# Kernel tuning notes

Hardware: AMD Instinct MI355X
Metric: run time of the kernel (lower is better)

## Reference

```python
import jax, jax.numpy as jnp
import numpy as np

B, C, H, NP, M = 32, 768, 12, 196, 64
D = C // H
GRID = 14  # sqrt(196)
NG = 1 + NP  # cls + patches = 197
EPS = 1e-5


def _ln(x, w, b):
    mu = x.mean(-1, keepdims=True)
    var = ((x - mu) ** 2).mean(-1, keepdims=True)
    return (x - mu) * jax.lax.rsqrt(var + EPS) * w + b


def setup_inputs() -> dict:
    key = jax.random.key(0)
    ks = jax.random.split(key, 14)
    std = 0.02
    return {
        "x": jax.random.normal(ks[0], (B, NG + M, C), dtype=jnp.float32),
        "ps": jax.random.uniform(ks[1], (B, M, 2), dtype=jnp.float32) * 224.0,
        "ns": jax.random.randint(ks[2], (B,), 1, M + 1, dtype=jnp.int32),
        "norm1_w": jnp.ones((C,), jnp.float32),
        "norm1_b": jnp.zeros((C,), jnp.float32),
        "qkv_w": jax.random.normal(ks[3], (3 * C, C), jnp.float32) * std,
        "proj_w": jax.random.normal(ks[4], (C, C), jnp.float32) * std,
        "proj_b": jnp.zeros((C,), jnp.float32),
        "norm2_w": jnp.ones((C,), jnp.float32),
        "norm2_b": jnp.zeros((C,), jnp.float32),
        "fc1_w": jax.random.normal(ks[5], (4 * C, C), jnp.float32) * std,
        "fc1_b": jnp.zeros((4 * C,), jnp.float32),
        "fc2_w": jax.random.normal(ks[6], (C, 4 * C), jnp.float32) * std,
        "fc2_b": jnp.zeros((C,), jnp.float32),
    }


def reference(x, ps, ns, norm1_w, norm1_b, qkv_w, proj_w, proj_b,
              norm2_w, norm2_b, fc1_w, fc1_b, fc2_w, fc2_b):
    Bn, Nt, Cd = x.shape  # Nt = 1 + 196 + M
    scale = D ** -0.5

    h = _ln(x, norm1_w, norm1_b)
    qkv = (h @ qkv_w.T).reshape(Bn, Nt, 3, H, D).transpose(2, 0, 3, 1, 4)  # [3,B,H,Nt,D]
    q, k, v = qkv[0], qkv[1], qkv[2]

    # ---- global attention over cls + patch tokens (first 197) ----
    attn = jnp.einsum('bhnd,bhmd->bhnm', q[:, :, :NG], k[:, :, :NG]) * scale
    attn = jax.nn.softmax(attn, axis=-1)
    xg = jnp.einsum('bhnm,bhmd->bhnd', attn, v[:, :, :NG])
    xg = xg.transpose(0, 2, 1, 3).reshape(Bn, NG, Cd)  # [B,197,C]

    # ---- keypoint bilinear-gather attention (get_single_filter_matrix) ----
    pos = ps / 16.0  # [B,M,2]; pos[...,1] -> row (dim 4), pos[...,0] -> col (dim 5)
    c0 = jnp.clip(jnp.floor(pos[..., 0]), 0, GRID - 1).astype(jnp.int32)
    c1 = jnp.clip(jnp.ceil(pos[..., 0]), 0, GRID - 1).astype(jnp.int32)
    r0 = jnp.clip(jnp.floor(pos[..., 1]), 0, GRID - 1).astype(jnp.int32)
    r1 = jnp.clip(jnp.ceil(pos[..., 1]), 0, GRID - 1).astype(jnp.int32)
    # neighbor order: top_left, top_right, bottom_left, bottom_right
    rows = jnp.stack([r0, r1, r0, r1], axis=-1)  # [B,M,4]
    cols = jnp.stack([c0, c0, c1, c1], axis=-1)
    flat = rows * GRID + cols  # [B,M,4] flat index into 196 patch tokens

    kp = k[:, :, 1:NG]  # [B,H,196,D]
    vp = v[:, :, 1:NG]
    idx = jnp.broadcast_to(flat.reshape(Bn, 1, M * 4, 1), (Bn, H, M * 4, D))
    knb = jnp.take_along_axis(kp, idx, axis=2).reshape(Bn, H, M, 4, D)
    vnb = jnp.take_along_axis(vp, idx, axis=2).reshape(Bn, H, M, 4, D)

    qk = q[:, :, NG:]  # keypoint queries [B,H,M,D]
    a = jnp.einsum('bhmd,bhmjd->bhmj', qk, knb)  # no scale, per original
    a = jax.nn.softmax(a, axis=-1)
    kout = jnp.einsum('bhmj,bhmjd->bhmd', a, vnb)
    kout = kout.transpose(0, 2, 1, 3).reshape(Bn, M, Cd)

    y = jnp.concatenate([xg, kout], axis=1) @ proj_w.T + proj_b
    x = x + y

    h2 = _ln(x, norm2_w, norm2_b)
    h2 = jax.nn.gelu(h2 @ fc1_w.T + fc1_b, approximate=False)
    x = x + (h2 @ fc2_w.T + fc2_b)
    return x
```

## Files before the change

### kernel.cpp

```cpp
#include <hip/hip_runtime.h>

typedef unsigned short u16;
typedef unsigned int u32;
typedef u16 u16x8 __attribute__((ext_vector_type(8)));
typedef u16 u16x4 __attribute__((ext_vector_type(4)));
typedef float f32x4 __attribute__((ext_vector_type(4)));
typedef __bf16 bf16x8 __attribute__((ext_vector_type(8)));

#define NHEAD 12
#define NT 261
#define NGL 197
#define CDIM 768
#define KT 14
#define PS_STRIDE 232
#define VT_STRIDE 232

__device__ __forceinline__ float bf2f(u16 u) {
    u32 x = ((u32)u) << 16;
    float f;
    __builtin_memcpy(&f, &x, 4);
    return f;
}
__device__ __forceinline__ u16 f2bf(float f) {
    u32 x;
    __builtin_memcpy(&x, &f, 4);
    x = (x + 0x7fffu + ((x >> 16) & 1u)) >> 16;
    return (u16)x;
}

#define GLD_LDS16(g, l) \
    __builtin_amdgcn_global_load_lds((const __attribute__((address_space(1))) void*)(g), \
                                     (__attribute__((address_space(3))) void*)(l), 16, 0, 0)
#define WAITV(n) asm volatile("s_waitcnt vmcnt(" #n ")" ::: "memory")
#define BARM() asm volatile("s_barrier" ::: "memory")

struct CvArgs {
    const float* in[4];
    u16* out[4];
    int n4[4];
};

__device__ __forceinline__ void ln_row(const float* __restrict__ in, const float* __restrict__ w,
                                       const float* __restrict__ bia, u16* __restrict__ out,
                                       int row, int lane) {
    const float4* r = (const float4*)(in + (size_t)row * CDIM);
    float4 a = r[lane], b4 = r[lane + 64], c4 = r[lane + 128];
    float s  = a.x + a.y + a.z + a.w + b4.x + b4.y + b4.z + b4.w + c4.x + c4.y + c4.z + c4.w;
    float ss = a.x*a.x + a.y*a.y + a.z*a.z + a.w*a.w
             + b4.x*b4.x + b4.y*b4.y + b4.z*b4.z + b4.w*b4.w
             + c4.x*c4.x + c4.y*c4.y + c4.z*c4.z + c4.w*c4.w;
#pragma unroll
    for (int off = 32; off; off >>= 1) {
        s  += __shfl_xor(s, off);
        ss += __shfl_xor(ss, off);
    }
    float mu = s * (1.f / 768.f);
    float var = ss * (1.f / 768.f) - mu * mu;
    float inv = rsqrtf(var + 1e-5f);
    const float4* wp = (const float4*)w;
    const float4* bp = (const float4*)bia;
    u16* o = out + (size_t)row * CDIM;
#pragma unroll
    for (int t = 0; t < 3; ++t) {
        float4 v = (t == 0) ? a : (t == 1) ? b4 : c4;
        float4 ww = wp[lane + t * 64], bb = bp[lane + t * 64];
        u16x4 ov;
        ov[0] = f2bf((v.x - mu) * inv * ww.x + bb.x);
        ov[1] = f2bf((v.y - mu) * inv * ww.y + bb.y);
        ov[2] = f2bf((v.z - mu) * inv * ww.z + bb.z);
        ov[3] = f2bf((v.w - mu) * inv * ww.w + bb.w);
        *(u16x4*)(o + t * 256 + lane * 4) = ov;
    }
}

__global__ __launch_bounds__(256) void pre_k(const float* __restrict__ x, const float* __restrict__ w,
                                             const float* __restrict__ bia, u16* __restrict__ out,
                                             int nrows, CvArgs cv) {
    if (blockIdx.y == 0) {
        int i = blockIdx.x * 256 + threadIdx.x;
        int s0 = cv.n4[0], s1 = s0 + cv.n4[1], s2 = s1 + cv.n4[2], s3 = s2 + cv.n4[3];
        const float* in;
        u16* o;
        int base;
        if (i < s0)      { in = cv.in[0]; o = cv.out[0]; base = 0; }
        else if (i < s1) { in = cv.in[1]; o = cv.out[1]; base = s0; }
        else if (i < s2) { in = cv.in[2]; o = cv.out[2]; base = s1; }
        else if (i < s3) { in = cv.in[3]; o = cv.out[3]; base = s2; }
        else return;
        int j = i - base;
        float4 v = ((const float4*)in)[j];
        u16x4 ov;
        ov[0] = f2bf(v.x); ov[1] = f2bf(v.y); ov[2] = f2bf(v.z); ov[3] = f2bf(v.w);
        ((u16x4*)o)[j] = ov;
    } else {
        int lane = threadIdx.x & 63, wv = threadIdx.x >> 6;
        int row = blockIdx.x * 4 + wv;
        if (row < nrows) ln_row(x, w, bia, out, row, lane);
    }
}

__global__ __launch_bounds__(256) void ln_w(const float* __restrict__ in, const float* __restrict__ w,
                                            const float* __restrict__ bia, u16* __restrict__ out, int nrows) {
    int lane = threadIdx.x & 63, wv = threadIdx.x >> 6;
    int row = blockIdx.x * 4 + wv;
    if (row < nrows) ln_row(in, w, bia, out, row, lane);
}

template <int EPI>
__global__ __launch_bounds__(512, 2) void gemm5(const u16* __restrict__ A, const u16* __restrict__ Bw,
                                                int M, int N, int K, int nbn,
                                                const float* __restrict__ bias,
                                                void* __restrict__ outp) {
    __shared__ __align__(16) u16 sm[2][32768];
    const int tid = threadIdx.x;
    const int nwg = gridDim.x;
    const int q = nwg >> 3, r = nwg & 7;
    const int xcd = blockIdx.x & 7, within = blockIdx.x >> 3;
    const int id2 = (xcd < r ? xcd * (q + 1) : r * (q + 1) + (xcd - r) * q) + within;
    const int bm = id2 / nbn, bn = id2 % nbn;
    const int lane = tid & 63, wv = tid >> 6;
    const int wr = wv >> 2, wc = wv & 3;
    const int l15 = lane & 15, lg = lane >> 4;
    const int arow0 = bm * 256, brow0 = bn * 256;
    const int nt = K >> 6;

    const int srow = tid >> 3;
    const int sk = ((tid & 7) ^ (srow & 7)) * 8;
    const u16* gA[4];
    const u16* gB[4];
#pragma unroll
    for (int i = 0; i < 4; ++i) {
        int ar = arow0 + i * 64 + srow;
        if (ar >= M) ar = M - 1;
        gA[i] = A + (size_t)ar * K + sk;
        gB[i] = Bw + (size_t)(brow0 + i * 64 + srow) * K + sk;
    }

    auto STAGE = [&](int tt) {
        u16* sb = sm[tt & 1];
        const size_t ko = (size_t)tt * 64;
#pragma unroll
        for (int i = 0; i < 4; ++i) GLD_LDS16(gA[i] + ko, sb + i * 4096 + tid * 8);
#pragma unroll
        for (int i = 0; i < 4; ++i) GLD_LDS16(gB[i] + ko, sb + 16384 + i * 4096 + tid * 8);
    };

    f32x4 acc[8][4] = {};
    const int xb = l15 & 7;

    STAGE(0);
    for (int t = 0; t < nt; ++t) {
        if (t + 1 < nt) {
            STAGE(t + 1);
            WAITV(8);
        } else {
            WAITV(0);
        }
        BARM();
        const u16* sb = sm[t & 1];
        bf16x8 bq[4][2];
#pragma unroll
        for (int ni = 0; ni < 4; ++ni)
#pragma unroll
            for (int kk = 0; kk < 2; ++kk)
                bq[ni][kk] = *(const bf16x8*)(sb + 16384 + (wc * 64 + ni * 16 + l15) * 64 + (((kk << 2) | lg) ^ xb) * 8);
#pragma unroll
        for (int mi = 0; mi < 8; ++mi) {
            const u16* arow = sb + (wr * 128 + mi * 16 + l15) * 64;
            bf16x8 a0 = *(const bf16x8*)(arow + ((lg ^ xb) * 8));
            bf16x8 a1 = *(const bf16x8*)(arow + (((4 | lg) ^ xb) * 8));
#pragma unroll
            for (int ni = 0; ni < 4; ++ni) {
                acc[mi][ni] = __builtin_amdgcn_mfma_f32_16x16x32_bf16(a0, bq[ni][0], acc[mi][ni], 0, 0, 0);
                acc[mi][ni] = __builtin_amdgcn_mfma_f32_16x16x32_bf16(a1, bq[ni][1], acc[mi][ni], 0, 0, 0);
            }
        }
        if (t + 2 < nt) BARM();
    }

#pragma unroll
    for (int mi = 0; mi < 8; ++mi) {
        int row0 = arow0 + wr * 128 + mi * 16 + lg * 4;
#pragma unroll
        for (int ni = 0; ni < 4; ++ni) {
            int col = brow0 + wc * 64 + ni * 16 + l15;
            float bb = (EPI == 0) ? 0.f : bias[col];
#pragma unroll
            for (int rr = 0; rr < 4; ++rr) {
                int row = row0 + rr;
                if (row < M) {
                    float v = acc[mi][ni][rr] + bb;
                    if (EPI == 2) {
                        float z = v + 0.044715f * v * v * v;
                        v = v / (1.f + __expf(-1.5957691216f * z));
                    }
                    ((u16*)outp)[(size_t)row * N + col] = f2bf(v);
                }
            }
        }
    }
}

__global__ __launch_bounds__(256, 2) void gemm4n(const u16* __restrict__ A, const u16* __restrict__ Bw,
                                                 int M, int N, int K, int nbn,
                                                 const float* __restrict__ bias,
                                                 const float* __restrict__ resid, void* __restrict__ outp) {
    constexpr int SLOT = 128 * 64 + 8192;
    __shared__ __align__(16) u16 sm[2 * SLOT];
    const int tid = threadIdx.x;
    const int nwg = gridDim.x;
    const int q = nwg >> 3, r = nwg & 7;
    const int xcd = blockIdx.x & 7, within = blockIdx.x >> 3;
    const int id2 = (xcd < r ? xcd * (q + 1) : r * (q + 1) + (xcd - r) * q) + within;
    const int bm = id2 / nbn, bn = id2 % nbn;
    const int lane = tid & 63, wv = tid >> 6;
    const int wr = wv >> 1, wc = wv & 1;
    const int l15 = lane & 15, lg = lane >> 4;
    const int arow0 = bm * 128, brow0 = bn * 128;
    const int nt = K >> 6;

    const int srow = tid >> 3;
    const int sk = ((tid & 7) ^ (srow & 7)) * 8;
    const u16* gA[4];
    const u16* gB[4];
#pragma unroll
    for (int i = 0; i < 4; ++i) {
        int ar = arow0 + i * 32 + srow;
        if (ar >= M) ar = M - 1;
        gA[i] = A + (size_t)ar * K + sk;
        gB[i] = Bw + (size_t)(brow0 + i * 32 + srow) * K + sk;
    }

    auto STAGE = [&](int tt) {
        u16* sb = sm + (tt & 1) * SLOT;
        const size_t ko = (size_t)tt * 64;
#pragma unroll
        for (int i = 0; i < 4; ++i) GLD_LDS16(gA[i] + ko, sb + i * 2048 + tid * 8);
#pragma unroll
        for (int i = 0; i < 4; ++i) GLD_LDS16(gB[i] + ko, sb + 8192 + i * 2048 + tid * 8);
    };

    f32x4 acc[4][4] = {};
    const int xb = l15 & 7;

    STAGE(0);
    for (int t = 0; t < nt; ++t) {
        if (t + 1 < nt) {
            STAGE(t + 1);
            WAITV(8);
        } else {
            WAITV(0);
        }
        BARM();
        const u16* sb = sm + (t & 1) * SLOT;
        bf16x8 af[4][2], bq[4][2];
#pragma unroll
        for (int mi = 0; mi < 4; ++mi)
#pragma unroll
            for (int kk = 0; kk < 2; ++kk)
                af[mi][kk] = *(const bf16x8*)(sb + (wr * 64 + mi * 16 + l15) * 64 + (((kk << 2) | lg) ^ xb) * 8);
#pragma unroll
        for (int ni = 0; ni < 4; ++ni)
#pragma unroll
            for (int kk = 0; kk < 2; ++kk)
                bq[ni][kk] = *(const bf16x8*)(sb + 8192 + (wc * 64 + ni * 16 + l15) * 64 + (((kk << 2) | lg) ^ xb) * 8);
#pragma unroll
        for (int mi = 0; mi < 4; ++mi)
#pragma unroll
            for (int ni = 0; ni < 4; ++ni) {
                acc[mi][ni] = __builtin_amdgcn_mfma_f32_16x16x32_bf16(af[mi][0], bq[ni][0], acc[mi][ni], 0, 0, 0);
                acc[mi][ni] = __builtin_amdgcn_mfma_f32_16x16x32_bf16(af[mi][1], bq[ni][1], acc[mi][ni], 0, 0, 0);
            }
        if (t + 2 < nt) BARM();
    }

#pragma unroll
    for (int mi = 0; mi < 4; ++mi) {
        int row0 = arow0 + wr * 64 + mi * 16 + lg * 4;
#pragma unroll
        for (int ni = 0; ni < 4; ++ni) {
            int col = brow0 + wc * 64 + ni * 16 + l15;
            float bb = bias[col];
#pragma unroll
            for (int rr = 0; rr < 4; ++rr) {
                int row = row0 + rr;
                if (row < M) {
                    float v = acc[mi][ni][rr] + bb + resid[(size_t)row * N + col];
                    ((float*)outp)[(size_t)row * N + col] = v;
                }
            }
        }
    }
}

__global__ __launch_bounds__(256) void attn_fused(const u16* __restrict__ qkv, const float* __restrict__ ps,
                                                  u16* __restrict__ Z) {
    __shared__ __align__(16) u16 lds0[4 * 16 * PS_STRIDE];
    __shared__ __align__(16) u16 Vt[64 * VT_STRIDE];
    const int tid = threadIdx.x;
    const int lane = tid & 63, wv = tid >> 6;

    if (blockIdx.x >= 1536) {
        int idx = blockIdx.x - 1536;
        int b = idx >> 4;
        int m = (idx & 15) * 4 + wv;
        float px = ps[((size_t)b * 64 + m) * 2 + 0] * (1.f / 16.f);
        float py = ps[((size_t)b * 64 + m) * 2 + 1] * (1.f / 16.f);
        int c0 = min(max((int)floorf(px), 0), 13);
        int c1 = min(max((int)ceilf(px), 0), 13);
        int r0 = min(max((int)floorf(py), 0), 13);
        int r1 = min(max((int)ceilf(py), 0), 13);
        int tok[4];
        tok[0] = 1 + r0 * 14 + c0;
        tok[1] = 1 + r1 * 14 + c0;
        tok[2] = 1 + r0 * 14 + c1;
        tok[3] = 1 + r1 * 14 + c1;
        const size_t rowq = ((size_t)b * NT + NGL + m) * 2304;
#pragma unroll 1
        for (int h = 0; h < NHEAD; ++h) {
            float qv = bf2f(qkv[rowq + h * 64 + lane]);
            float a[4];
#pragma unroll
            for (int j = 0; j < 4; ++j) {
                float p = qv * bf2f(qkv[((size_t)b * NT + tok[j]) * 2304 + 768 + h * 64 + lane]);
#pragma unroll
                for (int off = 32; off; off >>= 1) p += __shfl_xor(p, off);
                a[j] = p;
            }
            float mx = fmaxf(fmaxf(a[0], a[1]), fmaxf(a[2], a[3]));
            float e0 = expf(a[0] - mx), e1 = expf(a[1] - mx), e2 = expf(a[2] - mx), e3 = expf(a[3] - mx);
            float inv = 1.f / (e0 + e1 + e2 + e3);
            float v0 = bf2f(qkv[((size_t)b * NT + tok[0]) * 2304 + 1536 + h * 64 + lane]);
            float v1 = bf2f(qkv[((size_t)b * NT + tok[1]) * 2304 + 1536 + h * 64 + lane]);
            float v2 = bf2f(qkv[((size_t)b * NT + tok[2]) * 2304 + 1536 + h * 64 + lane]);
            float v3 = bf2f(qkv[((size_t)b * NT + tok[3]) * 2304 + 1536 + h * 64 + lane]);
            float o = (e0 * v0 + e1 * v1 + e2 * v2 + e3 * v3) * inv;
            Z[((size_t)b * NT + NGL + m) * CDIM + h * 64 + lane] = f2bf(o);
        }
        return;
    }

    const int blk = blockIdx.x;
    const int qt = blk & 3;
    const int bh = blk >> 2;
    const int h = bh % NHEAD, b = bh / NHEAD;
    const int l15 = lane & 15, lg = lane >> 4;
    const u16* base = qkv + (size_t)b * NT * 2304;

    for (int c = tid; c < 224 * 8; c += 256) {
        int row = c >> 3, ch = c & 7;
        u16x8 v = {};
        if (row < NGL) v = *(const u16x8*)(base + (size_t)row * 2304 + 768 + h * 64 + ch * 8);
        int byte = row * 128 + ((ch * 16) ^ ((row & 7) << 4));
        *(u16x8*)((char*)lds0 + byte) = v;
    }
    for (int c = tid; c < 112 * 8; c += 256) {
        int mp = c >> 3, dch = c & 7;
        int m0 = mp * 2;
        u16x8 a0 = {}, a1 = {};
        if (m0 < NGL)     a0 = *(const u16x8*)(base + (size_t)m0 * 2304 + 1536 + h * 64 + dch * 8);
        if (m0 + 1 < NGL) a1 = *(const u16x8*)(base + (size_t)(m0 + 1) * 2304 + 1536 + h * 64 + dch * 8);
#pragma unroll
        for (int j = 0; j < 8; ++j) {
            u32 pk = (u32)a0[j] | ((u32)a1[j] << 16);
            *(u32*)((char*)Vt + (size_t)(dch * 8 + j) * (VT_STRIDE * 2) + m0 * 2) = pk;
        }
    }
    const int q0 = qt * 64 + wv * 16;
    int qrow = q0 + l15; if (qrow > NGL - 1) qrow = NGL - 1;
    bf16x8 aq0 = *(const bf16x8*)(base + (size_t)qrow * 2304 + h * 64 + lg * 8);
    bf16x8 aq1 = *(const bf16x8*)(base + (size_t)qrow * 2304 + h * 64 + 32 + lg * 8);
    __syncthreads();

    f32x4 s[KT];
    const int sw = (l15 & 7) << 4;
#pragma unroll
    for (int t = 0; t < KT; ++t) {
        const char* krow = (const char*)lds0 + (t * 16 + l15) * 128;
        bf16x8 bk0 = *(const bf16x8*)(krow + ((lg * 16) ^ sw));
        bf16x8 bk1 = *(const bf16x8*)(krow + ((64 + lg * 16) ^ sw));
        f32x4 acc = {};
        acc = __builtin_amdgcn_mfma_f32_16x16x32_bf16(aq0, bk0, acc, 0, 0, 0);
        acc = __builtin_amdgcn_mfma_f32_16x16x32_bf16(aq1, bk1, acc, 0, 0, 0);
        s[t] = acc * 0.125f;
    }
    float mx[4] = {-1e30f, -1e30f, -1e30f, -1e30f};
#pragma unroll
    for (int t = 0; t < KT; ++t)
#pragma unroll
        for (int r = 0; r < 4; ++r) mx[r] = fmaxf(mx[r], s[t][r]);
#pragma unroll
    for (int off = 1; off < 16; off <<= 1)
#pragma unroll
        for (int r = 0; r < 4; ++r) mx[r] = fmaxf(mx[r], __shfl_xor(mx[r], off));
    float sum[4] = {};
#pragma unroll
    for (int t = 0; t < KT; ++t) {
        bool valid = (t * 16 + l15) < NGL;
#pragma unroll
        for (int r = 0; r < 4; ++r) {
            float e = valid ? __expf(s[t][r] - mx[r]) : 0.f;
            s[t][r] = e;
            sum[r] += e;
        }
    }
#pragma unroll
    for (int off = 1; off < 16; off <<= 1)
#pragma unroll
        for (int r = 0; r < 4; ++r) sum[r] += __shfl_xor(sum[r], off);
    float inv[4];
#pragma unroll
    for (int r = 0; r < 4; ++r) inv[r] = 1.f / sum[r];

    __syncthreads();
    u16* Pw = lds0 + wv * 16 * PS_STRIDE;
#pragma unroll
    for (int t = 0; t < KT; ++t)
#pragma unroll
        for (int r = 0; r < 4; ++r)
            Pw[(4 * lg + r) * PS_STRIDE + t * 16 + l15] = f2bf(s[t][r] * inv[r]);

    f32x4 o[4] = {};
#pragma unroll
    for (int ks = 0; ks < 7; ++ks) {
        bf16x8 pa = *(const bf16x8*)(Pw + l15 * PS_STRIDE + ks * 32 + lg * 8);
#pragma unroll
        for (int dt = 0; dt < 4; ++dt) {
            bf16x8 bv = *(const bf16x8*)((const char*)Vt + (size_t)(dt * 16 + l15) * (VT_STRIDE * 2) + ks * 64 + lg * 16);
            o[dt] = __builtin_amdgcn_mfma_f32_16x16x32_bf16(pa, bv, o[dt], 0, 0, 0);
        }
    }
#pragma unroll
    for (int dt = 0; dt < 4; ++dt)
#pragma unroll
        for (int r = 0; r < 4; ++r) {
            int q = q0 + 4 * lg + r;
            if (q < NGL) Z[((size_t)b * NT + q) * CDIM + h * 64 + dt * 16 + l15] = f2bf(o[dt][r]);
        }
}

extern "C" void kernel_launch(void* const* d_in, const int* in_sizes, int n_in,
                              void* d_out, int out_size, void* d_ws, size_t ws_size,
                              hipStream_t stream) {
    const float* x      = (const float*)d_in[0];
    const float* ps     = (const float*)d_in[1];
    const float* n1w    = (const float*)d_in[3];
    const float* n1b    = (const float*)d_in[4];
    const float* qkv_w  = (const float*)d_in[5];
    const float* proj_w = (const float*)d_in[6];
    const float* proj_b = (const float*)d_in[7];
    const float* n2w    = (const float*)d_in[8];
    const float* n2b    = (const float*)d_in[9];
    const float* fc1_w  = (const float*)d_in[10];
    const float* fc1_b  = (const float*)d_in[11];
    const float* fc2_w  = (const float*)d_in[12];
    const float* fc2_b  = (const float*)d_in[13];

    char* ws = (char*)d_ws;
    const int M = 32 * NT;
    u16* hbuf  = (u16*)ws;
    u16* qkvb  = (u16*)(ws + 12828672);
    u16* Zb    = (u16*)(ws + 12828672 + 38486016);
    u16* Gb    = (u16*)(ws + 12828672);
    float* x1  = (float*)(ws + 64143360);
    u16* wq    = (u16*)(ws + 89800704);
    u16* wp    = wq + 2304 * 768;
    u16* w1    = wp + 768 * 768;
    u16* w2    = w1 + 3072 * 768;

    CvArgs cv;
    cv.in[0] = qkv_w;  cv.out[0] = wq; cv.n4[0] = 2304 * 768 / 4;
    cv.in[1] = proj_w; cv.out[1] = wp; cv.n4[1] = 768 * 768 / 4;
    cv.in[2] = fc1_w;  cv.out[2] = w1; cv.n4[2] = 3072 * 768 / 4;
    cv.in[3] = fc2_w;  cv.out[3] = w2; cv.n4[3] = 768 * 3072 / 4;

    pre_k<<<dim3(6912, 2), 256, 0, stream>>>(x, n1w, n1b, hbuf, M, cv);
    gemm5<0><<<33 * 9, 512, 0, stream>>>(hbuf, wq, M, 2304, 768, 9, nullptr, qkvb);
    attn_fused<<<2048, 256, 0, stream>>>(qkvb, ps, Zb);
    gemm4n<<<66 * 6, 256, 0, stream>>>(Zb, wp, M, 768, 768, 6, proj_b, x, x1);
    ln_w<<<2088, 256, 0, stream>>>(x1, n2w, n2b, hbuf, M);
    gemm5<2><<<33 * 12, 512, 0, stream>>>(hbuf, w1, M, 3072, 768, 12, fc1_b, Gb);
    gemm4n<<<66 * 6, 256, 0, stream>>>(Gb, w2, M, 768, 3072, 6, fc2_b, x1, (float*)d_out);
}
```

Baseline: 302.0 us.

## Split GEMM main loop into four interleaved load/MFMA phases with priority hints

Restructures the 256x256 bf16 GEMM main loop into four quadrant phases. Each phase issues a slice of the next tile's global-to-LDS loads, reads part of the A/B fragments from LDS, and runs a quarter of the MFMAs under raised wave priority. The aim is to spread memory traffic across the compute and overlap LDS reads with MFMA work, in the style of ping-pong scheduling. The cost is many more barriers per iteration, and the finer-grained waits could serialize warps if the phases are unbalanced.

```diff
diff --git a/kernel.cpp b/kernel.cpp
--- a/kernel.cpp
+++ b/kernel.cpp
@@ -32,6 +32,7 @@
     __builtin_amdgcn_global_load_lds((const __attribute__((address_space(1))) void*)(g), \
                                      (__attribute__((address_space(3))) void*)(l), 16, 0, 0)
 #define WAITV(n) asm volatile("s_waitcnt vmcnt(" #n ")" ::: "memory")
+#define LGKM0() do { asm volatile("s_waitcnt lgkmcnt(0)" ::: "memory"); __builtin_amdgcn_sched_barrier(0); } while (0)
 #define BARM() asm volatile("s_barrier" ::: "memory")
 
 struct CvArgs {
@@ -107,7 +108,7 @@
 }
 
 template <int EPI>
-__global__ __launch_bounds__(512, 2) void gemm5(const u16* __restrict__ A, const u16* __restrict__ Bw,
+__global__ __launch_bounds__(512, 2) void gemm8(const u16* __restrict__ A, const u16* __restrict__ Bw,
                                                 int M, int N, int K, int nbn,
                                                 const float* __restrict__ bias,
                                                 void* __restrict__ outp) {
@@ -136,46 +137,114 @@
         gB[i] = Bw + (size_t)(brow0 + i * 64 + srow) * K + sk;
     }
 
-    auto STAGE = [&](int tt) {
-        u16* sb = sm[tt & 1];
-        const size_t ko = (size_t)tt * 64;
-#pragma unroll
-        for (int i = 0; i < 4; ++i) GLD_LDS16(gA[i] + ko, sb + i * 4096 + tid * 8);
-#pragma unroll
-        for (int i = 0; i < 4; ++i) GLD_LDS16(gB[i] + ko, sb + 16384 + i * 4096 + tid * 8);
-    };
-
     f32x4 acc[8][4] = {};
     const int xb = l15 & 7;
-
-    STAGE(0);
+    const int lds_tid = tid * 8;
+
+    {
+        u16* nb = sm[0];
+#pragma unroll
+        for (int i = 0; i < 4; ++i) GLD_LDS16(gA[i], nb + i * 4096 + lds_tid);
+#pragma unroll
+        for (int i = 0; i < 4; ++i) GLD_LDS16(gB[i], nb + 16384 + i * 4096 + lds_tid);
+    }
+
     for (int t = 0; t < nt; ++t) {
-        if (t + 1 < nt) {
-            STAGE(t + 1);
-            WAITV(8);
+        const u16* sb = sm[t & 1];
+        u16* nb = sm[(t & 1) ^ 1];
+        const bool pre = (t + 1 < nt);
+        const size_t ko = (size_t)(t + 1) * 64;
+        bf16x8 aLo[4][2], aHi[4][2], bLo[2][2], bHi[2][2];
+
+        if (pre) {
+            GLD_LDS16(gA[0] + ko, nb + 0 * 4096 + lds_tid);
+            GLD_LDS16(gA[1] + ko, nb + 1 * 4096 + lds_tid);
+            WAITV(2);
         } else {
             WAITV(0);
         }
         BARM();
-        const u16* sb = sm[t & 1];
-        bf16x8 bq[4][2];
-#pragma unroll
-        for (int ni = 0; ni < 4; ++ni)
+#pragma unroll
+        for (int mi = 0; mi < 4; ++mi)
 #pragma unroll
             for (int kk = 0; kk < 2; ++kk)
-                bq[ni][kk] = *(const bf16x8*)(sb + 16384 + (wc * 64 + ni * 16 + l15) * 64 + (((kk << 2) | lg) ^ xb) * 8);
-#pragma unroll
-        for (int mi = 0; mi < 8; ++mi) {
-            const u16* arow = sb + (wr * 128 + mi * 16 + l15) * 64;
-            bf16x8 a0 = *(const bf16x8*)(arow + ((lg ^ xb) * 8));
-            bf16x8 a1 = *(const bf16x8*)(arow + (((4 | lg) ^ xb) * 8));
-#pragma unroll
-            for (int ni = 0; ni < 4; ++ni) {
-                acc[mi][ni] = __builtin_amdgcn_mfma_f32_16x16x32_bf16(a0, bq[ni][0], acc[mi][ni], 0, 0, 0);
-                acc[mi][ni] = __builtin_amdgcn_mfma_f32_16x16x32_bf16(a1, bq[ni][1], acc[mi][ni], 0, 0, 0);
-            }
-        }
-        if (t + 2 < nt) BARM();
+                aLo[mi][kk] = *(const bf16x8*)(sb + (wr * 128 + mi * 16 + l15) * 64 + (((kk << 2) | lg) ^ xb) * 8);
+#pragma unroll
+        for (int ni = 0; ni < 2; ++ni)
+#pragma unroll
+            for (int kk = 0; kk < 2; ++kk)
+                bLo[ni][kk] = *(const bf16x8*)(sb + 16384 + (wc * 64 + ni * 16 + l15) * 64 + (((kk << 2) | lg) ^ xb) * 8);
+        LGKM0();
+        __builtin_amdgcn_s_setprio(1);
+#pragma unroll
+        for (int mi = 0; mi < 4; ++mi)
+#pragma unroll
+            for (int ni = 0; ni < 2; ++ni) {
+                acc[mi][ni] = __builtin_amdgcn_mfma_f32_16x16x32_bf16(aLo[mi][0], bLo[ni][0], acc[mi][ni], 0, 0, 0);
+                acc[mi][ni] = __builtin_amdgcn_mfma_f32_16x16x32_bf16(aLo[mi][1], bLo[ni][1], acc[mi][ni], 0, 0, 0);
+            }
+        __builtin_amdgcn_s_setprio(0);
+        BARM();
+
+        if (pre) {
+            GLD_LDS16(gA[2] + ko, nb + 2 * 4096 + lds_tid);
+            GLD_LDS16(gA[3] + ko, nb + 3 * 4096 + lds_tid);
+        }
+#pragma unroll
+        for (int ni = 0; ni < 2; ++ni)
+#pragma unroll
+            for (int kk = 0; kk < 2; ++kk)
+                bHi[ni][kk] = *(const bf16x8*)(sb + 16384 + (wc * 64 + (ni + 2) * 16 + l15) * 64 + (((kk << 2) | lg) ^ xb) * 8);
+        BARM();
+        LGKM0();
+        __builtin_amdgcn_s_setprio(1);
+#pragma unroll
+        for (int mi = 0; mi < 4; ++mi)
+#pragma unroll
+            for (int ni = 0; ni < 2; ++ni) {
+                acc[mi][ni + 2] = __builtin_amdgcn_mfma_f32_16x16x32_bf16(aLo[mi][0], bHi[ni][0], acc[mi][ni + 2], 0, 0, 0);
+                acc[mi][ni + 2] = __builtin_amdgcn_mfma_f32_16x16x32_bf16(aLo[mi][1], bHi[ni][1], acc[mi][ni + 2], 0, 0, 0);
+            }
+        __builtin_amdgcn_s_setprio(0);
+        BARM();
+
+        if (pre) {
+            GLD_LDS16(gB[0] + ko, nb + 16384 + 0 * 4096 + lds_tid);
+            GLD_LDS16(gB[1] + ko, nb + 16384 + 1 * 4096 + lds_tid);
+        }
+#pragma unroll
+        for (int mi = 0; mi < 4; ++mi)
+#pragma unroll
+            for (int kk = 0; kk < 2; ++kk)
+                aHi[mi][kk] = *(const bf16x8*)(sb + (wr * 128 + (mi + 4) * 16 + l15) * 64 + (((kk << 2) | lg) ^ xb) * 8);
+        BARM();
+        LGKM0();
+        __builtin_amdgcn_s_setprio(1);
+#pragma unroll
+        for (int mi = 0; mi < 4; ++mi)
+#pragma unroll
+            for (int ni = 0; ni < 2; ++ni) {
+                acc[mi + 4][ni + 2] = __builtin_amdgcn_mfma_f32_16x16x32_bf16(aHi[mi][0], bHi[ni][0], acc[mi + 4][ni + 2], 0, 0, 0);
+                acc[mi + 4][ni + 2] = __builtin_amdgcn_mfma_f32_16x16x32_bf16(aHi[mi][1], bHi[ni][1], acc[mi + 4][ni + 2], 0, 0, 0);
+            }
+        __builtin_amdgcn_s_setprio(0);
+        BARM();
+
+        if (pre) {
+            GLD_LDS16(gB[2] + ko, nb + 16384 + 2 * 4096 + lds_tid);
+            GLD_LDS16(gB[3] + ko, nb + 16384 + 3 * 4096 + lds_tid);
+        }
+        BARM();
+        __builtin_amdgcn_s_setprio(1);
+#pragma unroll
+        for (int mi = 0; mi < 4; ++mi)
+#pragma unroll
+            for (int ni = 0; ni < 2; ++ni) {
+                acc[mi + 4][ni] = __builtin_amdgcn_mfma_f32_16x16x32_bf16(aHi[mi][0], bLo[ni][0], acc[mi + 4][ni], 0, 0, 0);
+                acc[mi + 4][ni] = __builtin_amdgcn_mfma_f32_16x16x32_bf16(aHi[mi][1], bLo[ni][1], acc[mi + 4][ni], 0, 0, 0);
+            }
+        __builtin_amdgcn_s_setprio(0);
+        BARM();
     }
 
 #pragma unroll
@@ -475,10 +544,10 @@
     cv.in[3] = fc2_w;  cv.out[3] = w2; cv.n4[3] = 768 * 3072 / 4;
 
     pre_k<<<dim3(6912, 2), 256, 0, stream>>>(x, n1w, n1b, hbuf, M, cv);
-    gemm5<0><<<33 * 9, 512, 0, stream>>>(hbuf, wq, M, 2304, 768, 9, nullptr, qkvb);
+    gemm8<0><<<33 * 9, 512, 0, stream>>>(hbuf, wq, M, 2304, 768, 9, nullptr, qkvb);
     attn_fused<<<2048, 256, 0, stream>>>(qkvb, ps, Zb);
     gemm4n<<<66 * 6, 256, 0, stream>>>(Zb, wp, M, 768, 768, 6, proj_b, x, x1);
     ln_w<<<2088, 256, 0, stream>>>(x1, n2w, n2b, hbuf, M);
-    gemm5<2><<<33 * 12, 512, 0, stream>>>(hbuf, w1, M, 3072, 768, 12, fc1_b, Gb);
+    gemm8<2><<<33 * 12, 512, 0, stream>>>(hbuf, w1, M, 3072, 768, 12, fc1_b, Gb);
     gemm4n<<<66 * 6, 256, 0, stream>>>(Gb, w2, M, 768, 3072, 6, fc2_b, x1, (float*)d_out);
 }
```

New measurement: 301.9 us. No clear change (-0.0%).

## Pre-pack weights into MFMA fragment layout and load B directly to registers

Applied to the files above, without the earlier changes.

The weight conversion kernel now writes bf16 weights in a tiled layout that matches the 16x32 MFMA B-fragment. All four GEMMs then load B fragments straight from global memory into registers, so only A is staged through LDS. The main loop is unrolled by two with register double-buffering of B. This cuts LDS traffic and LDS footprint, but each wave now loads B independently from global or L2, so the same B data is fetched more times. It also adds a scheduling barrier after each vmcnt wait.

```diff
diff --git a/kernel.cpp b/kernel.cpp
--- a/kernel.cpp
+++ b/kernel.cpp
@@ -27,17 +27,23 @@
     x = (x + 0x7fffu + ((x >> 16) & 1u)) >> 16;
     return (u16)x;
 }
+__device__ __forceinline__ bf16x8 asbf(u16x8 v) {
+    bf16x8 r;
+    __builtin_memcpy(&r, &v, 16);
+    return r;
+}
 
 #define GLD_LDS16(g, l) \
     __builtin_amdgcn_global_load_lds((const __attribute__((address_space(1))) void*)(g), \
                                      (__attribute__((address_space(3))) void*)(l), 16, 0, 0)
-#define WAITV(n) asm volatile("s_waitcnt vmcnt(" #n ")" ::: "memory")
+#define WAITV(n) do { asm volatile("s_waitcnt vmcnt(" #n ")" ::: "memory"); __builtin_amdgcn_sched_barrier(0); } while (0)
 #define BARM() asm volatile("s_barrier" ::: "memory")
 
 struct CvArgs {
     const float* in[4];
     u16* out[4];
-    int n4[4];
+    int n8[4];
+    int K[4];
 };
 
 __device__ __forceinline__ void ln_row(const float* __restrict__ in, const float* __restrict__ w,
@@ -78,20 +84,27 @@
                                              int nrows, CvArgs cv) {
     if (blockIdx.y == 0) {
         int i = blockIdx.x * 256 + threadIdx.x;
-        int s0 = cv.n4[0], s1 = s0 + cv.n4[1], s2 = s1 + cv.n4[2], s3 = s2 + cv.n4[3];
-        const float* in;
-        u16* o;
-        int base;
-        if (i < s0)      { in = cv.in[0]; o = cv.out[0]; base = 0; }
-        else if (i < s1) { in = cv.in[1]; o = cv.out[1]; base = s0; }
-        else if (i < s2) { in = cv.in[2]; o = cv.out[2]; base = s1; }
-        else if (i < s3) { in = cv.in[3]; o = cv.out[3]; base = s2; }
+        int s0 = cv.n8[0], s1 = s0 + cv.n8[1], s2 = s1 + cv.n8[2], s3 = s2 + cv.n8[3];
+        int seg, base;
+        if (i < s0)      { seg = 0; base = 0; }
+        else if (i < s1) { seg = 1; base = s0; }
+        else if (i < s2) { seg = 2; base = s1; }
+        else if (i < s3) { seg = 3; base = s2; }
         else return;
         int j = i - base;
-        float4 v = ((const float4*)in)[j];
-        u16x4 ov;
-        ov[0] = f2bf(v.x); ov[1] = f2bf(v.y); ov[2] = f2bf(v.z); ov[3] = f2bf(v.w);
-        ((u16x4*)o)[j] = ov;
+        int Kd = cv.K[seg];
+        int kd8 = Kd >> 3;
+        int n = j / kd8;
+        int k8 = j - n * kd8;
+        const float* src = cv.in[seg] + (size_t)n * Kd + k8 * 8;
+        float4 v0 = *(const float4*)src;
+        float4 v1 = *(const float4*)(src + 4);
+        u16x8 ov;
+        ov[0] = f2bf(v0.x); ov[1] = f2bf(v0.y); ov[2] = f2bf(v0.z); ov[3] = f2bf(v0.w);
+        ov[4] = f2bf(v1.x); ov[5] = f2bf(v1.y); ov[6] = f2bf(v1.z); ov[7] = f2bf(v1.w);
+        int chunk = (n >> 4) * (Kd >> 5) + (k8 >> 2);
+        int dst = chunk * 512 + ((k8 & 3) * 16 + (n & 15)) * 8;
+        *(u16x8*)(cv.out[seg] + dst) = ov;
     } else {
         int lane = threadIdx.x & 63, wv = threadIdx.x >> 6;
         int row = blockIdx.x * 4 + wv;
@@ -107,11 +120,10 @@
 }
 
 template <int EPI>
-__global__ __launch_bounds__(512, 2) void gemm5(const u16* __restrict__ A, const u16* __restrict__ Bw,
-                                                int M, int N, int K, int nbn,
-                                                const float* __restrict__ bias,
-                                                void* __restrict__ outp) {
-    __shared__ __align__(16) u16 sm[2][32768];
+__global__ __launch_bounds__(512) void gemm9(const u16* __restrict__ A, const u16* __restrict__ Bp,
+                                             int M, int N, int K, int nbn,
+                                             const float* __restrict__ bias, void* __restrict__ outp) {
+    __shared__ __align__(16) u16 smA[2][16384];
     const int tid = threadIdx.x;
     const int nwg = gridDim.x;
     const int q = nwg >> 3, r = nwg & 7;
@@ -123,47 +135,38 @@
     const int l15 = lane & 15, lg = lane >> 4;
     const int arow0 = bm * 256, brow0 = bn * 256;
     const int nt = K >> 6;
+    const int kch = K >> 5;
 
     const int srow = tid >> 3;
     const int sk = ((tid & 7) ^ (srow & 7)) * 8;
     const u16* gA[4];
-    const u16* gB[4];
 #pragma unroll
     for (int i = 0; i < 4; ++i) {
         int ar = arow0 + i * 64 + srow;
         if (ar >= M) ar = M - 1;
         gA[i] = A + (size_t)ar * K + sk;
-        gB[i] = Bw + (size_t)(brow0 + i * 64 + srow) * K + sk;
-    }
-
-    auto STAGE = [&](int tt) {
-        u16* sb = sm[tt & 1];
+    }
+    const u16* gBw = Bp + ((size_t)((brow0 >> 4) + wc * 4)) * kch * 512 + lane * 8;
+
+    auto STAGE_A = [&](int tt) {
+        u16* sb = smA[tt & 1];
         const size_t ko = (size_t)tt * 64;
 #pragma unroll
         for (int i = 0; i < 4; ++i) GLD_LDS16(gA[i] + ko, sb + i * 4096 + tid * 8);
-#pragma unroll
-        for (int i = 0; i < 4; ++i) GLD_LDS16(gB[i] + ko, sb + 16384 + i * 4096 + tid * 8);
     };
 
     f32x4 acc[8][4] = {};
     const int xb = l15 & 7;
-
-    STAGE(0);
-    for (int t = 0; t < nt; ++t) {
-        if (t + 1 < nt) {
-            STAGE(t + 1);
-            WAITV(8);
-        } else {
-            WAITV(0);
-        }
-        BARM();
-        const u16* sb = sm[t & 1];
-        bf16x8 bq[4][2];
+    u16x8 BqA[8], BqB[8];
+
+    auto LOADB = [&](u16x8* dst, int tt) {
 #pragma unroll
         for (int ni = 0; ni < 4; ++ni)
 #pragma unroll
             for (int kk = 0; kk < 2; ++kk)
-                bq[ni][kk] = *(const bf16x8*)(sb + 16384 + (wc * 64 + ni * 16 + l15) * 64 + (((kk << 2) | lg) ^ xb) * 8);
+                dst[ni * 2 + kk] = *(const u16x8*)(gBw + ((size_t)ni * kch + 2 * tt + kk) * 512);
+    };
+    auto COMPUTE = [&](const u16* sb, const u16x8* Bq) {
 #pragma unroll
         for (int mi = 0; mi < 8; ++mi) {
             const u16* arow = sb + (wr * 128 + mi * 16 + l15) * 64;
@@ -171,11 +174,34 @@
             bf16x8 a1 = *(const bf16x8*)(arow + (((4 | lg) ^ xb) * 8));
 #pragma unroll
             for (int ni = 0; ni < 4; ++ni) {
-                acc[mi][ni] = __builtin_amdgcn_mfma_f32_16x16x32_bf16(a0, bq[ni][0], acc[mi][ni], 0, 0, 0);
-                acc[mi][ni] = __builtin_amdgcn_mfma_f32_16x16x32_bf16(a1, bq[ni][1], acc[mi][ni], 0, 0, 0);
+                acc[mi][ni] = __builtin_amdgcn_mfma_f32_16x16x32_bf16(a0, asbf(Bq[ni * 2]), acc[mi][ni], 0, 0, 0);
+                acc[mi][ni] = __builtin_amdgcn_mfma_f32_16x16x32_bf16(a1, asbf(Bq[ni * 2 + 1]), acc[mi][ni], 0, 0, 0);
             }
         }
-        if (t + 2 < nt) BARM();
+    };
+
+    STAGE_A(0);
+    LOADB(BqA, 0);
+    for (int t = 0; t < nt; t += 2) {
+        STAGE_A(t + 1);
+        LOADB(BqB, t + 1);
+        WAITV(12);
+        BARM();
+        COMPUTE(smA[0], BqA);
+        if (t + 2 < nt) {
+            BARM();
+            STAGE_A(t + 2);
+            LOADB(BqA, t + 2);
+            WAITV(12);
+            BARM();
+            COMPUTE(smA[1], BqB);
+            BARM();
+        } else {
+            BARM();
+            WAITV(0);
+            BARM();
+            COMPUTE(smA[1], BqB);
+        }
     }
 
 #pragma unroll
@@ -201,12 +227,11 @@
     }
 }
 
-__global__ __launch_bounds__(256, 2) void gemm4n(const u16* __restrict__ A, const u16* __restrict__ Bw,
-                                                 int M, int N, int K, int nbn,
-                                                 const float* __restrict__ bias,
-                                                 const float* __restrict__ resid, void* __restrict__ outp) {
-    constexpr int SLOT = 128 * 64 + 8192;
-    __shared__ __align__(16) u16 sm[2 * SLOT];
+__global__ __launch_bounds__(256) void gemm9n(const u16* __restrict__ A, const u16* __restrict__ Bp,
+                                              int M, int N, int K, int nbn,
+                                              const float* __restrict__ bias,
+                                              const float* __restrict__ resid, void* __restrict__ outp) {
+    __shared__ __align__(16) u16 smA[2][8192];
     const int tid = threadIdx.x;
     const int nwg = gridDim.x;
     const int q = nwg >> 3, r = nwg & 7;
@@ -218,60 +243,73 @@
     const int l15 = lane & 15, lg = lane >> 4;
     const int arow0 = bm * 128, brow0 = bn * 128;
     const int nt = K >> 6;
+    const int kch = K >> 5;
 
     const int srow = tid >> 3;
     const int sk = ((tid & 7) ^ (srow & 7)) * 8;
     const u16* gA[4];
-    const u16* gB[4];
 #pragma unroll
     for (int i = 0; i < 4; ++i) {
         int ar = arow0 + i * 32 + srow;
         if (ar >= M) ar = M - 1;
         gA[i] = A + (size_t)ar * K + sk;
-        gB[i] = Bw + (size_t)(brow0 + i * 32 + srow) * K + sk;
-    }
-
-    auto STAGE = [&](int tt) {
-        u16* sb = sm + (tt & 1) * SLOT;
+    }
+    const u16* gBw = Bp + ((size_t)((brow0 >> 4) + wc * 4)) * kch * 512 + lane * 8;
+
+    auto STAGE_A = [&](int tt) {
+        u16* sb = smA[tt & 1];
         const size_t ko = (size_t)tt * 64;
 #pragma unroll
         for (int i = 0; i < 4; ++i) GLD_LDS16(gA[i] + ko, sb + i * 2048 + tid * 8);
-#pragma unroll
-        for (int i = 0; i < 4; ++i) GLD_LDS16(gB[i] + ko, sb + 8192 + i * 2048 + tid * 8);
     };
 
     f32x4 acc[4][4] = {};
     const int xb = l15 & 7;
-
-    STAGE(0);
-    for (int t = 0; t < nt; ++t) {
-        if (t + 1 < nt) {
-            STAGE(t + 1);
-            WAITV(8);
+    u16x8 BqA[8], BqB[8];
+
+    auto LOADB = [&](u16x8* dst, int tt) {
+#pragma unroll
+        for (int ni = 0; ni < 4; ++ni)
+#pragma unroll
+            for (int kk = 0; kk < 2; ++kk)
+                dst[ni * 2 + kk] = *(const u16x8*)(gBw + ((size_t)ni * kch + 2 * tt + kk) * 512);
+    };
+    auto COMPUTE = [&](const u16* sb, const u16x8* Bq) {
+#pragma unroll
+        for (int mi = 0; mi < 4; ++mi) {
+            const u16* arow = sb + (wr * 64 + mi * 16 + l15) * 64;
+            bf16x8 a0 = *(const bf16x8*)(arow + ((lg ^ xb) * 8));
+            bf16x8 a1 = *(const bf16x8*)(arow + (((4 | lg) ^ xb) * 8));
+#pragma unroll
+            for (int ni = 0; ni < 4; ++ni) {
+                acc[mi][ni] = __builtin_amdgcn_mfma_f32_16x16x32_bf16(a0, asbf(Bq[ni * 2]), acc[mi][ni], 0, 0, 0);
+                acc[mi][ni] = __builtin_amdgcn_mfma_f32_16x16x32_bf16(a1, asbf(Bq[ni * 2 + 1]), acc[mi][ni], 0, 0, 0);
+            }
+        }
+    };
+
+    STAGE_A(0);
+    LOADB(BqA, 0);
+    for (int t = 0; t < nt; t += 2) {
+        STAGE_A(t + 1);
+        LOADB(BqB, t + 1);
+        WAITV(12);
+        BARM();
+        COMPUTE(smA[0], BqA);
+        if (t + 2 < nt) {
+            BARM();
+            STAGE_A(t + 2);
+            LOADB(BqA, t + 2);
+            WAITV(12);
+            BARM();
+            COMPUTE(smA[1], BqB);
+            BARM();
         } else {
+            BARM();
             WAITV(0);
-        }
-        BARM();
-        const u16* sb = sm + (t & 1) * SLOT;
-        bf16x8 af[4][2], bq[4][2];
-#pragma unroll
-        for (int mi = 0; mi < 4; ++mi)
-#pragma unroll
-            for (int kk = 0; kk < 2; ++kk)
-                af[mi][kk] = *(const bf16x8*)(sb + (wr * 64 + mi * 16 + l15) * 64 + (((kk << 2) | lg) ^ xb) * 8);
-#pragma unroll
-        for (int ni = 0; ni < 4; ++ni)
-#pragma unroll
-            for (int kk = 0; kk < 2; ++kk)
-                bq[ni][kk] = *(const bf16x8*)(sb + 8192 + (wc * 64 + ni * 16 + l15) * 64 + (((kk << 2) | lg) ^ xb) * 8);
-#pragma unroll
-        for (int mi = 0; mi < 4; ++mi)
-#pragma unroll
-            for (int ni = 0; ni < 4; ++ni) {
-                acc[mi][ni] = __builtin_amdgcn_mfma_f32_16x16x32_bf16(af[mi][0], bq[ni][0], acc[mi][ni], 0, 0, 0);
-                acc[mi][ni] = __builtin_amdgcn_mfma_f32_16x16x32_bf16(af[mi][1], bq[ni][1], acc[mi][ni], 0, 0, 0);
-            }
-        if (t + 2 < nt) BARM();
+            BARM();
+            COMPUTE(smA[1], BqB);
+        }
     }
 
 #pragma unroll
@@ -469,16 +507,16 @@
     u16* w2    = w1 + 3072 * 768;
 
     CvArgs cv;
-    cv.in[0] = qkv_w;  cv.out[0] = wq; cv.n4[0] = 2304 * 768 / 4;
-    cv.in[1] = proj_w; cv.out[1] = wp; cv.n4[1] = 768 * 768 / 4;
-    cv.in[2] = fc1_w;  cv.out[2] = w1; cv.n4[2] = 3072 * 768 / 4;
-    cv.in[3] = fc2_w;  cv.out[3] = w2; cv.n4[3] = 768 * 3072 / 4;
-
-    pre_k<<<dim3(6912, 2), 256, 0, stream>>>(x, n1w, n1b, hbuf, M, cv);
-    gemm5<0><<<33 * 9, 512, 0, stream>>>(hbuf, wq, M, 2304, 768, 9, nullptr, qkvb);
+    cv.in[0] = qkv_w;  cv.out[0] = wq; cv.n8[0] = 2304 * 768 / 8; cv.K[0] = 768;
+    cv.in[1] = proj_w; cv.out[1] = wp; cv.n8[1] = 768 * 768 / 8;  cv.K[1] = 768;
+    cv.in[2] = fc1_w;  cv.out[2] = w1; cv.n8[2] = 3072 * 768 / 8; cv.K[2] = 768;
+    cv.in[3] = fc2_w;  cv.out[3] = w2; cv.n8[3] = 768 * 3072 / 8; cv.K[3] = 3072;
+
+    pre_k<<<dim3(3456, 2), 256, 0, stream>>>(x, n1w, n1b, hbuf, M, cv);
+    gemm9<0><<<33 * 9, 512, 0, stream>>>(hbuf, wq, M, 2304, 768, 9, nullptr, qkvb);
     attn_fused<<<2048, 256, 0, stream>>>(qkvb, ps, Zb);
-    gemm4n<<<66 * 6, 256, 0, stream>>>(Zb, wp, M, 768, 768, 6, proj_b, x, x1);
+    gemm9n<<<66 * 6, 256, 0, stream>>>(Zb, wp, M, 768, 768, 6, proj_b, x, x1);
     ln_w<<<2088, 256, 0, stream>>>(x1, n2w, n2b, hbuf, M);
-    gemm5<2><<<33 * 12, 512, 0, stream>>>(hbuf, w1, M, 3072, 768, 12, fc1_b, Gb);
-    gemm4n<<<66 * 6, 256, 0, stream>>>(Gb, w2, M, 768, 3072, 6, fc2_b, x1, (float*)d_out);
-}
+    gemm9<2><<<33 * 12, 512, 0, stream>>>(hbuf, w1, M, 3072, 768, 12, fc1_b, Gb);
+    gemm9n<<<66 * 6, 256, 0, stream>>>(Gb, w2, M, 768, 3072, 6, fc2_b, x1, (float*)d_out);
+}
```

Result: slower. 688.7 us (+128.1%).

## Unify GEMMs into one 128x128 kernel with K=32 stages and higher occupancy

Applied to the files above, without the earlier changes.

Replaces the 256x256 gemm5 and the K=64 gemm4n with a single templated gemm11 that uses 128x128 tiles and K-steps of 32, a 4-slot swizzle, and 32 KB of LDS so four blocks fit per CU. QKV and FC1 now launch many more, smaller workgroups (18 and 24 column tiles), and the epilogue variants (plain, GELU, bias plus residual) are merged behind a template parameter. The aim is better CU fill and latency hiding through more resident waves. The cost is lower per-tile data reuse and twice as many barrier and wait steps per unit of K.

```diff
diff --git a/kernel.cpp b/kernel.cpp
--- a/kernel.cpp
+++ b/kernel.cpp
@@ -107,106 +107,11 @@
 }
 
 template <int EPI>
-__global__ __launch_bounds__(512, 2) void gemm5(const u16* __restrict__ A, const u16* __restrict__ Bw,
-                                                int M, int N, int K, int nbn,
-                                                const float* __restrict__ bias,
-                                                void* __restrict__ outp) {
-    __shared__ __align__(16) u16 sm[2][32768];
-    const int tid = threadIdx.x;
-    const int nwg = gridDim.x;
-    const int q = nwg >> 3, r = nwg & 7;
-    const int xcd = blockIdx.x & 7, within = blockIdx.x >> 3;
-    const int id2 = (xcd < r ? xcd * (q + 1) : r * (q + 1) + (xcd - r) * q) + within;
-    const int bm = id2 / nbn, bn = id2 % nbn;
-    const int lane = tid & 63, wv = tid >> 6;
-    const int wr = wv >> 2, wc = wv & 3;
-    const int l15 = lane & 15, lg = lane >> 4;
-    const int arow0 = bm * 256, brow0 = bn * 256;
-    const int nt = K >> 6;
-
-    const int srow = tid >> 3;
-    const int sk = ((tid & 7) ^ (srow & 7)) * 8;
-    const u16* gA[4];
-    const u16* gB[4];
-#pragma unroll
-    for (int i = 0; i < 4; ++i) {
-        int ar = arow0 + i * 64 + srow;
-        if (ar >= M) ar = M - 1;
-        gA[i] = A + (size_t)ar * K + sk;
-        gB[i] = Bw + (size_t)(brow0 + i * 64 + srow) * K + sk;
-    }
-
-    auto STAGE = [&](int tt) {
-        u16* sb = sm[tt & 1];
-        const size_t ko = (size_t)tt * 64;
-#pragma unroll
-        for (int i = 0; i < 4; ++i) GLD_LDS16(gA[i] + ko, sb + i * 4096 + tid * 8);
-#pragma unroll
-        for (int i = 0; i < 4; ++i) GLD_LDS16(gB[i] + ko, sb + 16384 + i * 4096 + tid * 8);
-    };
-
-    f32x4 acc[8][4] = {};
-    const int xb = l15 & 7;
-
-    STAGE(0);
-    for (int t = 0; t < nt; ++t) {
-        if (t + 1 < nt) {
-            STAGE(t + 1);
-            WAITV(8);
-        } else {
-            WAITV(0);
-        }
-        BARM();
-        const u16* sb = sm[t & 1];
-        bf16x8 bq[4][2];
-#pragma unroll
-        for (int ni = 0; ni < 4; ++ni)
-#pragma unroll
-            for (int kk = 0; kk < 2; ++kk)
-                bq[ni][kk] = *(const bf16x8*)(sb + 16384 + (wc * 64 + ni * 16 + l15) * 64 + (((kk << 2) | lg) ^ xb) * 8);
-#pragma unroll
-        for (int mi = 0; mi < 8; ++mi) {
-            const u16* arow = sb + (wr * 128 + mi * 16 + l15) * 64;
-            bf16x8 a0 = *(const bf16x8*)(arow + ((lg ^ xb) * 8));
-            bf16x8 a1 = *(const bf16x8*)(arow + (((4 | lg) ^ xb) * 8));
-#pragma unroll
-            for (int ni = 0; ni < 4; ++ni) {
-                acc[mi][ni] = __builtin_amdgcn_mfma_f32_16x16x32_bf16(a0, bq[ni][0], acc[mi][ni], 0, 0, 0);
-                acc[mi][ni] = __builtin_amdgcn_mfma_f32_16x16x32_bf16(a1, bq[ni][1], acc[mi][ni], 0, 0, 0);
-            }
-        }
-        if (t + 2 < nt) BARM();
-    }
-
-#pragma unroll
-    for (int mi = 0; mi < 8; ++mi) {
-        int row0 = arow0 + wr * 128 + mi * 16 + lg * 4;
-#pragma unroll
-        for (int ni = 0; ni < 4; ++ni) {
-            int col = brow0 + wc * 64 + ni * 16 + l15;
-            float bb = (EPI == 0) ? 0.f : bias[col];
-#pragma unroll
-            for (int rr = 0; rr < 4; ++rr) {
-                int row = row0 + rr;
-                if (row < M) {
-                    float v = acc[mi][ni][rr] + bb;
-                    if (EPI == 2) {
-                        float z = v + 0.044715f * v * v * v;
-                        v = v / (1.f + __expf(-1.5957691216f * z));
-                    }
-                    ((u16*)outp)[(size_t)row * N + col] = f2bf(v);
-                }
-            }
-        }
-    }
-}
-
-__global__ __launch_bounds__(256, 2) void gemm4n(const u16* __restrict__ A, const u16* __restrict__ Bw,
+__global__ __launch_bounds__(256, 4) void gemm11(const u16* __restrict__ A, const u16* __restrict__ Bw,
                                                  int M, int N, int K, int nbn,
                                                  const float* __restrict__ bias,
                                                  const float* __restrict__ resid, void* __restrict__ outp) {
-    constexpr int SLOT = 128 * 64 + 8192;
-    __shared__ __align__(16) u16 sm[2 * SLOT];
+    __shared__ __align__(16) u16 sm[2][8192];
     const int tid = threadIdx.x;
     const int nwg = gridDim.x;
     const int q = nwg >> 3, r = nwg & 7;
@@ -217,60 +122,55 @@
     const int wr = wv >> 1, wc = wv & 1;
     const int l15 = lane & 15, lg = lane >> 4;
     const int arow0 = bm * 128, brow0 = bn * 128;
-    const int nt = K >> 6;
-
-    const int srow = tid >> 3;
-    const int sk = ((tid & 7) ^ (srow & 7)) * 8;
-    const u16* gA[4];
-    const u16* gB[4];
-#pragma unroll
-    for (int i = 0; i < 4; ++i) {
-        int ar = arow0 + i * 32 + srow;
+    const int nt = K >> 5;
+
+    const int srow = tid >> 2;
+    const int sslot = tid & 3;
+    const int sk = (sslot ^ ((srow >> 1) & 3)) * 8;
+    const u16* gA[2];
+    const u16* gB[2];
+#pragma unroll
+    for (int i = 0; i < 2; ++i) {
+        int ar = arow0 + i * 64 + srow;
         if (ar >= M) ar = M - 1;
         gA[i] = A + (size_t)ar * K + sk;
-        gB[i] = Bw + (size_t)(brow0 + i * 32 + srow) * K + sk;
+        gB[i] = Bw + (size_t)(brow0 + i * 64 + srow) * K + sk;
     }
 
     auto STAGE = [&](int tt) {
-        u16* sb = sm + (tt & 1) * SLOT;
-        const size_t ko = (size_t)tt * 64;
-#pragma unroll
-        for (int i = 0; i < 4; ++i) GLD_LDS16(gA[i] + ko, sb + i * 2048 + tid * 8);
-#pragma unroll
-        for (int i = 0; i < 4; ++i) GLD_LDS16(gB[i] + ko, sb + 8192 + i * 2048 + tid * 8);
+        u16* sb = sm[tt & 1];
+        const size_t ko = (size_t)tt * 32;
+#pragma unroll
+        for (int i = 0; i < 2; ++i) GLD_LDS16(gA[i] + ko, sb + i * 2048 + tid * 8);
+#pragma unroll
+        for (int i = 0; i < 2; ++i) GLD_LDS16(gB[i] + ko, sb + 4096 + i * 2048 + tid * 8);
     };
 
     f32x4 acc[4][4] = {};
-    const int xb = l15 & 7;
+    const int xb = (l15 >> 1) & 3;
 
     STAGE(0);
     for (int t = 0; t < nt; ++t) {
         if (t + 1 < nt) {
             STAGE(t + 1);
-            WAITV(8);
+            WAITV(4);
         } else {
             WAITV(0);
         }
         BARM();
-        const u16* sb = sm + (t & 1) * SLOT;
-        bf16x8 af[4][2], bq[4][2];
+        const u16* sb = sm[t & 1];
+        bf16x8 af[4], bq[4];
 #pragma unroll
         for (int mi = 0; mi < 4; ++mi)
-#pragma unroll
-            for (int kk = 0; kk < 2; ++kk)
-                af[mi][kk] = *(const bf16x8*)(sb + (wr * 64 + mi * 16 + l15) * 64 + (((kk << 2) | lg) ^ xb) * 8);
+            af[mi] = *(const bf16x8*)(sb + (wr * 64 + mi * 16 + l15) * 32 + ((lg ^ xb) * 8));
 #pragma unroll
         for (int ni = 0; ni < 4; ++ni)
-#pragma unroll
-            for (int kk = 0; kk < 2; ++kk)
-                bq[ni][kk] = *(const bf16x8*)(sb + 8192 + (wc * 64 + ni * 16 + l15) * 64 + (((kk << 2) | lg) ^ xb) * 8);
+            bq[ni] = *(const bf16x8*)(sb + 4096 + (wc * 64 + ni * 16 + l15) * 32 + ((lg ^ xb) * 8));
 #pragma unroll
         for (int mi = 0; mi < 4; ++mi)
 #pragma unroll
-            for (int ni = 0; ni < 4; ++ni) {
-                acc[mi][ni] = __builtin_amdgcn_mfma_f32_16x16x32_bf16(af[mi][0], bq[ni][0], acc[mi][ni], 0, 0, 0);
-                acc[mi][ni] = __builtin_amdgcn_mfma_f32_16x16x32_bf16(af[mi][1], bq[ni][1], acc[mi][ni], 0, 0, 0);
-            }
+            for (int ni = 0; ni < 4; ++ni)
+                acc[mi][ni] = __builtin_amdgcn_mfma_f32_16x16x32_bf16(af[mi], bq[ni], acc[mi][ni], 0, 0, 0);
         if (t + 2 < nt) BARM();
     }
 
@@ -280,13 +180,22 @@
 #pragma unroll
         for (int ni = 0; ni < 4; ++ni) {
             int col = brow0 + wc * 64 + ni * 16 + l15;
-            float bb = bias[col];
+            float bb = (EPI == 0) ? 0.f : bias[col];
 #pragma unroll
             for (int rr = 0; rr < 4; ++rr) {
                 int row = row0 + rr;
                 if (row < M) {
-                    float v = acc[mi][ni][rr] + bb + resid[(size_t)row * N + col];
-                    ((float*)outp)[(size_t)row * N + col] = v;
+                    float v = acc[mi][ni][rr] + bb;
+                    if (EPI == 2) {
+                        float z = v + 0.044715f * v * v * v;
+                        v = v / (1.f + __expf(-1.5957691216f * z));
+                    }
+                    if (EPI == 1) {
+                        v += resid[(size_t)row * N + col];
+                        ((float*)outp)[(size_t)row * N + col] = v;
+                    } else {
+                        ((u16*)outp)[(size_t)row * N + col] = f2bf(v);
+                    }
                 }
             }
         }
@@ -475,10 +384,10 @@
     cv.in[3] = fc2_w;  cv.out[3] = w2; cv.n4[3] = 768 * 3072 / 4;
 
     pre_k<<<dim3(6912, 2), 256, 0, stream>>>(x, n1w, n1b, hbuf, M, cv);
-    gemm5<0><<<33 * 9, 512, 0, stream>>>(hbuf, wq, M, 2304, 768, 9, nullptr, qkvb);
+    gemm11<0><<<66 * 18, 256, 0, stream>>>(hbuf, wq, M, 2304, 768, 18, nullptr, nullptr, qkvb);
     attn_fused<<<2048, 256, 0, stream>>>(qkvb, ps, Zb);
-    gemm4n<<<66 * 6, 256, 0, stream>>>(Zb, wp, M, 768, 768, 6, proj_b, x, x1);
+    gemm11<1><<<66 * 6, 256, 0, stream>>>(Zb, wp, M, 768, 768, 6, proj_b, x, x1);
     ln_w<<<2088, 256, 0, stream>>>(x1, n2w, n2b, hbuf, M);
-    gemm5<2><<<33 * 12, 512, 0, stream>>>(hbuf, w1, M, 3072, 768, 12, fc1_b, Gb);
-    gemm4n<<<66 * 6, 256, 0, stream>>>(Gb, w2, M, 768, 3072, 6, fc2_b, x1, (float*)d_out);
-}
+    gemm11<2><<<66 * 24, 256, 0, stream>>>(hbuf, w1, M, 3072, 768, 24, fc1_b, nullptr, Gb);
+    gemm11<1><<<66 * 6, 256, 0, stream>>>(Gb, w2, M, 768, 3072, 6, fc2_b, x1, (float*)d_out);
+}
```

After: 280.8 us. -7.0%, faster.
